# Optimization experiments

Hardware: AMD Instinct MI355X
Metric: run time of the kernel (lower is better)

Reference implementation:

```python
import jax, jax.numpy as jnp
import numpy as np

K = 7  # hardcoded pooling grid in the module


def setup_inputs() -> dict:
    key = jax.random.key(0)
    k1, k2, k3, k4, k5 = jax.random.split(key, 5)
    B, C1, H, W = 4, 21, 100, 100
    cls_conv_out = jax.random.normal(k1, (B, C1 * K * K, H, W), dtype=jnp.float32)
    n = 2000
    # ROIs: (ymin, xmin, ymax, xmax) integer coords; spans >= K so bin steps >= 1
    ymin = jax.random.randint(k2, (n,), 0, 40)
    ylen = jax.random.randint(k3, (n,), K, 57)
    xmin = jax.random.randint(k4, (n,), 0, 40)
    xlen = jax.random.randint(k5, (n,), K, 57)
    rois = jnp.stack([ymin, xmin, ymin + ylen, xmin + xlen], axis=1).astype(jnp.int32)
    return {"cls_conv_out": cls_conv_out, "rois": rois}


def _ps_roi_pool(cls_conv_out, rois):
    k = K
    B, C, H, W = cls_conv_out.shape
    c1 = C // (k * k)
    # Original indexes batch element `_ - 1` where `_` is the batch size -> last element.
    # Channel ordering from the `count` counter: channel = (j*k + l)*c1 + cls.
    feat = cls_conv_out[B - 1].reshape(k, k, c1, H, W)
    # Integral image (summed-area table) so each variable-size bin mean is 4 gathers.
    I = jnp.pad(feat, ((0, 0), (0, 0), (0, 0), (1, 0), (1, 0))).cumsum(axis=3).cumsum(axis=4)  # [k,k,c1,H+1,W+1]

    ymin, xmin, ymax, xmax = rois[:, 0], rois[:, 1], rois[:, 2], rois[:, 3]
    ys = (ymax - ymin) // k  # per-ROI bin step (int floor, as in int(range/k))
    xs = (xmax - xmin) // k
    j = jnp.arange(k)
    y0 = ymin[:, None] + j[None, :] * ys[:, None]  # [n,k] bin starts
    y1 = y0 + ys[:, None]                          # [n,k] bin stops
    x0 = xmin[:, None] + j[None, :] * xs[:, None]
    x1 = x0 + xs[:, None]

    jj = j[None, :, None, None]
    ll = j[None, None, :, None]
    cc = jnp.arange(c1)[None, None, None, :]
    Y0 = y0[:, :, None, None]; Y1 = y1[:, :, None, None]
    X0 = x0[:, None, :, None]; X1 = x1[:, None, :, None]
    # bin sums via SAT: [n, k, k, c1]
    S = (I[jj, ll, cc, Y1, X1] - I[jj, ll, cc, Y0, X1]
         - I[jj, ll, cc, Y1, X0] + I[jj, ll, cc,0*Y0 + Y0, X0])
    area = (ys * xs).astype(S.dtype)[:, None, None, None]
    pooled = S / area  # per-bin mean -> pooling_track, layout [n,k,k,c1]
    return pooled


def reference(cls_conv_out, rois):
    pooled = _ps_roi_pool(cls_conv_out, rois)          # [n,k,k,c1]
    avg = pooled.mean(axis=(1, 2))                     # AvgPool2d((7,7)) -> [n,c1]
    # nn.Softmax() on a 4D tensor applies over dim=1 (classes)
    scores = jax.nn.softmax(avg, axis=1)[:, :, None, None]  # [n,c1,1,1]
    return scores
```

## Files before the change

kernel.cpp:

```cpp
#include <hip/hip_runtime.h>
#include <math.h>

#define KK      7
#define C1      21
#define NPLANES (KK * KK * C1)
#define H       100
#define W       100

__global__ __launch_bounds__(256) void plane_partial(
    const float* __restrict__ src,
    size_t batch_off,
    const int*  __restrict__ rois,
    int nrois,
    float* __restrict__ partial)
{
    const int p  = blockIdx.x;
    const int jl = p / C1;
    const int l  = jl % KK;
    const int j  = jl / KK;
    const int t  = threadIdx.x;

    __shared__ float tile[H * W];

    {
        const float4* p4 = (const float4*)(src + batch_off + (size_t)p * (H * W));
        float4* t4 = (float4*)tile;
        for (int i = t; i < (H * W) / 4; i += 256) t4[i] = p4[i];
    }
    __syncthreads();

    if (t < H) {
        float s = 0.f;
        int base = t * W;
        for (int x = 0; x < W; ++x) { s += tile[base + x]; tile[base + x] = s; }
    }
    __syncthreads();

    if (t < W) {
        float s = 0.f;
        for (int y = 0; y < H; ++y) { s += tile[y * W + t]; tile[y * W + t] = s; }
    }
    __syncthreads();

    float* prow = partial + (size_t)p * nrois;
    for (int n = t; n < nrois; n += 256) {
        const int4 r  = ((const int4*)rois)[n];
        const int ys  = (r.z - r.x) / KK;
        const int xs  = (r.w - r.y) / KK;
        const int y0  = r.x + j * ys;
        const int x0  = r.y + l * xs;
        const int y1  = y0 + ys - 1;
        const int x1  = x0 + xs - 1;

        float S = tile[y1 * W + x1];
        if (x0 > 0)           S -= tile[y1 * W + (x0 - 1)];
        if (y0 > 0)           S -= tile[(y0 - 1) * W + x1];
        if (y0 > 0 && x0 > 0) S += tile[(y0 - 1) * W + (x0 - 1)];

        prow[n] = S;
    }
}

__global__ __launch_bounds__(256) void reduce_chan(
    const float* __restrict__ partial,
    int nrois,
    float* __restrict__ chansum)
{
    const int c = blockIdx.y;
    const int n = blockIdx.x * 256 + threadIdx.x;
    if (n >= nrois) return;

    float s = 0.f;
    for (int jl = 0; jl < KK * KK; ++jl) {
        s += partial[(size_t)(jl * C1 + c) * nrois + n];
    }
    chansum[(size_t)n * C1 + c] = s;
}

__global__ __launch_bounds__(256) void softmax_out(
    const float* __restrict__ chansum,
    const int*   __restrict__ rois,
    int nrois,
    float*       __restrict__ out)
{
    const int n = blockIdx.x * 256 + threadIdx.x;
    if (n >= nrois) return;

    const int4 r  = ((const int4*)rois)[n];
    const int ys  = (r.z - r.x) / KK;
    const int xs  = (r.w - r.y) / KK;
    const float inv = 1.0f / (49.0f * (float)(ys * xs));

    float v[C1];
    float m = -INFINITY;
    #pragma unroll
    for (int c = 0; c < C1; ++c) {
        v[c] = chansum[(size_t)n * C1 + c] * inv;
        m = fmaxf(m, v[c]);
    }
    float s = 0.f;
    #pragma unroll
    for (int c = 0; c < C1; ++c) { v[c] = __expf(v[c] - m); s += v[c]; }
    const float rs = 1.0f / s;
    #pragma unroll
    for (int c = 0; c < C1; ++c) out[(size_t)n * C1 + c] = v[c] * rs;
}

__global__ __launch_bounds__(256) void roi_pool_direct(
    const float* __restrict__ src,
    size_t batch_off,
    const int*   __restrict__ rois,
    float*       __restrict__ out)
{
    const int n = blockIdx.x;
    const int t = threadIdx.x;

    __shared__ float chsum[C1];
    if (t < C1) chsum[t] = 0.f;
    __syncthreads();

    const int ymin = rois[4 * n + 0];
    const int xmin = rois[4 * n + 1];
    const int ymax = rois[4 * n + 2];
    const int xmax = rois[4 * n + 3];
    const int ys = (ymax - ymin) / KK;
    const int xs = (xmax - xmin) / KK;

    const float* base = src + batch_off;

    for (int idx = t; idx < NPLANES; idx += blockDim.x) {
        const int c  = idx % C1;
        const int jl = idx / C1;
        const int l  = jl % KK;
        const int j  = jl / KK;
        const int y0 = ymin + j * ys;
        const int x0 = xmin + l * xs;
        const float* plane = base + (size_t)idx * (H * W);
        float s = 0.f;
        for (int y = y0; y < y0 + ys; ++y) {
            const float* row = plane + (size_t)y * W + x0;
            for (int x = 0; x < xs; ++x) s += row[x];
        }
        atomicAdd(&chsum[c], s);
    }
    __syncthreads();

    if (t == 0) {
        const float inv = 1.0f / (49.0f * (float)(ys * xs));
        float m = -INFINITY;
        float v[C1];
        for (int c = 0; c < C1; ++c) { v[c] = chsum[c] * inv; m = fmaxf(m, v[c]); }
        float s = 0.f;
        for (int c = 0; c < C1; ++c) { v[c] = expf(v[c] - m); s += v[c]; }
        const float rs = 1.0f / s;
        for (int c = 0; c < C1; ++c) out[(size_t)n * C1 + c] = v[c] * rs;
    }
}

extern "C" void kernel_launch(void* const* d_in, const int* in_sizes, int n_in,
                              void* d_out, int out_size, void* d_ws, size_t ws_size,
                              hipStream_t stream)
{
    const float* cls  = (const float*)d_in[0];
    const int*   rois = (const int*)d_in[1];
    float*       out  = (float*)d_out;

    const int nrois = in_sizes[1] / 4;
    const size_t plane_elems = (size_t)NPLANES * H * W;
    const int B = (int)((size_t)in_sizes[0] / plane_elems);
    const size_t batch_off = (size_t)(B - 1) * plane_elems;

    const size_t partial_bytes = (size_t)NPLANES * nrois * sizeof(float);
    const size_t chansum_off   = (partial_bytes + 255) & ~(size_t)255;
    const size_t need = chansum_off + (size_t)nrois * C1 * sizeof(float);

    if (ws_size >= need) {
        float* partial = (float*)d_ws;
        float* chansum = (float*)((char*)d_ws + chansum_off);

        plane_partial<<<NPLANES, 256, 0, stream>>>(cls, batch_off, rois, nrois, partial);

        dim3 rgrid((nrois + 255) / 256, C1);
        reduce_chan<<<rgrid, 256, 0, stream>>>(partial, nrois, chansum);

        softmax_out<<<(nrois + 255) / 256, 256, 0, stream>>>(chansum, rois, nrois, out);
    } else {
        roi_pool_direct<<<nrois, 256, 0, stream>>>(cls, batch_off, rois, out);
    }
}
```

Baseline: 223.4 us.

## Pad shared SAT tile stride and fuse channel reduction with softmax

The shared-memory integral-image tile now uses a row stride of 101 instead of 100. This is meant to reduce LDS bank conflicts in the column prefix-sum pass and the ROI corner lookups, at the cost of scalar stores during the tile load. The separate channel-reduction and softmax kernels are merged into one kernel that processes 16 ROIs per block, staging channel sums in shared memory. That removes a launch and the chansum workspace round trip, but leaves fewer active threads during the softmax phase.

After: 218.8 us. 1.02x faster.

```diff
diff --git a/kernel.cpp b/kernel.cpp
--- a/kernel.cpp
+++ b/kernel.cpp
@@ -6,6 +6,7 @@
 #define NPLANES (KK * KK * C1)
 #define H       100
 #define W       100
+#define TS      101
 
 __global__ __launch_bounds__(256) void plane_partial(
     const float* __restrict__ src,
@@ -20,25 +21,30 @@
     const int j  = jl / KK;
     const int t  = threadIdx.x;
 
-    __shared__ float tile[H * W];
+    __shared__ float tile[H * TS];
 
     {
         const float4* p4 = (const float4*)(src + batch_off + (size_t)p * (H * W));
-        float4* t4 = (float4*)tile;
-        for (int i = t; i < (H * W) / 4; i += 256) t4[i] = p4[i];
+        for (int i = t; i < (H * W) / 4; i += 256) {
+            float4 v = p4[i];
+            int g = i * 4;
+            int y = g / W, x = g - y * W;
+            float* d = &tile[y * TS + x];
+            d[0] = v.x; d[1] = v.y; d[2] = v.z; d[3] = v.w;
+        }
     }
     __syncthreads();
 
     if (t < H) {
         float s = 0.f;
-        int base = t * W;
-        for (int x = 0; x < W; ++x) { s += tile[base + x]; tile[base + x] = s; }
+        float* row = &tile[t * TS];
+        for (int x = 0; x < W; ++x) { s += row[x]; row[x] = s; }
     }
     __syncthreads();
 
     if (t < W) {
         float s = 0.f;
-        for (int y = 0; y < H; ++y) { s += tile[y * W + t]; tile[y * W + t] = s; }
+        for (int y = 0; y < H; ++y) { s += tile[y * TS + t]; tile[y * TS + t] = s; }
     }
     __syncthreads();
 
@@ -52,58 +58,65 @@
         const int y1  = y0 + ys - 1;
         const int x1  = x0 + xs - 1;
 
-        float S = tile[y1 * W + x1];
-        if (x0 > 0)           S -= tile[y1 * W + (x0 - 1)];
-        if (y0 > 0)           S -= tile[(y0 - 1) * W + x1];
-        if (y0 > 0 && x0 > 0) S += tile[(y0 - 1) * W + (x0 - 1)];
+        float S = tile[y1 * TS + x1];
+        if (x0 > 0)           S -= tile[y1 * TS + (x0 - 1)];
+        if (y0 > 0)           S -= tile[(y0 - 1) * TS + x1];
+        if (y0 > 0 && x0 > 0) S += tile[(y0 - 1) * TS + (x0 - 1)];
 
         prow[n] = S;
     }
 }
 
-__global__ __launch_bounds__(256) void reduce_chan(
+#define RB 16
+
+__global__ __launch_bounds__(256) void reduce_softmax(
     const float* __restrict__ partial,
-    int nrois,
-    float* __restrict__ chansum)
-{
-    const int c = blockIdx.y;
-    const int n = blockIdx.x * 256 + threadIdx.x;
-    if (n >= nrois) return;
-
-    float s = 0.f;
-    for (int jl = 0; jl < KK * KK; ++jl) {
-        s += partial[(size_t)(jl * C1 + c) * nrois + n];
-    }
-    chansum[(size_t)n * C1 + c] = s;
-}
-
-__global__ __launch_bounds__(256) void softmax_out(
-    const float* __restrict__ chansum,
     const int*   __restrict__ rois,
     int nrois,
     float*       __restrict__ out)
 {
-    const int n = blockIdx.x * 256 + threadIdx.x;
-    if (n >= nrois) return;
+    const int dn = threadIdx.x & (RB - 1);
+    const int cg = threadIdx.x / RB;
+    const int n  = blockIdx.x * RB + dn;
 
-    const int4 r  = ((const int4*)rois)[n];
-    const int ys  = (r.z - r.x) / KK;
-    const int xs  = (r.w - r.y) / KK;
-    const float inv = 1.0f / (49.0f * (float)(ys * xs));
+    __shared__ float ch[RB][C1];
 
-    float v[C1];
-    float m = -INFINITY;
-    #pragma unroll
-    for (int c = 0; c < C1; ++c) {
-        v[c] = chansum[(size_t)n * C1 + c] * inv;
-        m = fmaxf(m, v[c]);
+    if (n < nrois) {
+        for (int c = cg; c < C1; c += 16) {
+            float s = 0.f;
+            const float* pc = partial + (size_t)c * nrois + n;
+            #pragma unroll
+            for (int jl = 0; jl < KK * KK; ++jl) {
+                s += pc[(size_t)jl * C1 * nrois];
+            }
+            ch[dn][c] = s;
+        }
     }
-    float s = 0.f;
-    #pragma unroll
-    for (int c = 0; c < C1; ++c) { v[c] = __expf(v[c] - m); s += v[c]; }
-    const float rs = 1.0f / s;
-    #pragma unroll
-    for (int c = 0; c < C1; ++c) out[(size_t)n * C1 + c] = v[c] * rs;
+    __syncthreads();
+
+    if (threadIdx.x < RB) {
+        const int n2 = blockIdx.x * RB + threadIdx.x;
+        if (n2 < nrois) {
+            const int4 r  = ((const int4*)rois)[n2];
+            const int ys  = (r.z - r.x) / KK;
+            const int xs  = (r.w - r.y) / KK;
+            const float inv = 1.0f / (49.0f * (float)(ys * xs));
+
+            float v[C1];
+            float m = -INFINITY;
+            #pragma unroll
+            for (int c = 0; c < C1; ++c) {
+                v[c] = ch[threadIdx.x][c] * inv;
+                m = fmaxf(m, v[c]);
+            }
+            float s = 0.f;
+            #pragma unroll
+            for (int c = 0; c < C1; ++c) { v[c] = __expf(v[c] - m); s += v[c]; }
+            const float rs = 1.0f / s;
+            #pragma unroll
+            for (int c = 0; c < C1; ++c) out[(size_t)n2 * C1 + c] = v[c] * rs;
+        }
+    }
 }
 
 __global__ __launch_bounds__(256) void roi_pool_direct(
@@ -170,20 +183,11 @@
     const int B = (int)((size_t)in_sizes[0] / plane_elems);
     const size_t batch_off = (size_t)(B - 1) * plane_elems;
 
-    const size_t partial_bytes = (size_t)NPLANES * nrois * sizeof(float);
-    const size_t chansum_off   = (partial_bytes + 255) & ~(size_t)255;
-    const size_t need = chansum_off + (size_t)nrois * C1 * sizeof(float);
-
+    const size_t need = (size_t)NPLANES * nrois * sizeof(float);
     if (ws_size >= need) {
         float* partial = (float*)d_ws;
-        float* chansum = (float*)((char*)d_ws + chansum_off);
-
         plane_partial<<<NPLANES, 256, 0, stream>>>(cls, batch_off, rois, nrois, partial);
-
-        dim3 rgrid((nrois + 255) / 256, C1);
-        reduce_chan<<<rgrid, 256, 0, stream>>>(partial, nrois, chansum);
-
-        softmax_out<<<(nrois + 255) / 256, 256, 0, stream>>>(chansum, rois, nrois, out);
+        reduce_softmax<<<(nrois + RB - 1) / RB, 256, 0, stream>>>(partial, rois, nrois, out);
     } else {
         roi_pool_direct<<<nrois, 256, 0, stream>>>(cls, batch_off, rois, out);
     }
```
